# Kernel optimization log

Hardware: AMD Instinct MI355X
Metric: run time of the kernel (lower is better)

## Reference

```python
import jax, jax.numpy as jnp
import numpy as np

B, T, H, NH = 4, 4096, 768, 12
D = H          # attention inner dim (expand_ratio = 1)
I = 4 * H      # MLP intermediate size


def rms_norm(x, eps=1e-6):
    return x * jax.lax.rsqrt(jnp.mean(x * x, axis=-1, keepdims=True) + eps)


def layer_norm(x, eps=1e-6):
    mu = jnp.mean(x, axis=-1, keepdims=True)
    var = jnp.mean((x - mu) ** 2, axis=-1, keepdims=True)
    return (x - mu) * jax.lax.rsqrt(var + eps)


def act_quant(x):
    # per-token int8 absmax quantization (BitNet b1.58)
    scale = 127.0 / jnp.maximum(jnp.max(jnp.abs(x), axis=-1, keepdims=True), 1e-5)
    return jnp.clip(jnp.round(x * scale), -128, 127) / scale


def weight_quant(w):
    # per-tensor ternary quantization
    scale = 1.0 / jnp.maximum(jnp.mean(jnp.abs(w)), 1e-5)
    return jnp.clip(jnp.round(w * scale), -1, 1) / scale


def bit_linear(x, w, b=None):
    xn = rms_norm(x)
    xq = xn + jax.lax.stop_gradient(act_quant(xn) - xn)  # STE
    wq = w + jax.lax.stop_gradient(weight_quant(w) - w)  # STE
    y = jnp.einsum('...k,nk->...n', xq, wq)
    return y if b is None else y + b


def setup_inputs() -> dict:
    key = jax.random.key(0)
    ks = jax.random.split(key, 12)
    s = 0.02
    return dict(
        x=jax.random.normal(ks[0], (B, T, H), jnp.float32),
        c=jax.random.normal(ks[1], (B, H), jnp.float32),
        w_emb=jax.random.normal(ks[2], (2 * H, H), jnp.float32) * s,
        b_emb=jnp.zeros((2 * H,), jnp.float32),
        w_i=jax.random.normal(ks[3], (D, H), jnp.float32) * s,
        w_f=jax.random.normal(ks[4], (D, H), jnp.float32) * s,
        w_g=jax.random.normal(ks[5], (D, H), jnp.float32) * s,
        w_gn=jnp.ones((D,), jnp.float32),
        w_o=jax.random.normal(ks[6], (H, D), jnp.float32) * s,
        w_gate=jax.random.normal(ks[7], (2 * I, H), jnp.float32) * s,
        w_down=jax.random.normal(ks[8], (H, I), jnp.float32) * s,
        w_proj=jax.random.normal(ks[9], (H, 2 * H), jnp.float32) * s,
        b_proj=jnp.zeros((H,), jnp.float32),
    )


def reference(x, c, w_emb, b_emb, w_i, w_f, w_g, w_gn, w_o,
              w_gate, w_down, w_proj, b_proj):
    # --- AdaLayerNormZeroSingle ---
    emb = jnp.einsum('bk,nk->bn', jax.nn.silu(c), w_emb) + b_emb   # [B, 2H]
    scale, gate = jnp.split(emb, 2, axis=-1)                        # [B, H] each
    nx = layer_norm(x) * (1.0 + scale[:, None, :])                  # [B, T, H]

    # --- HGRNBitAttention: gated elementwise linear recurrence ---
    i = bit_linear(nx, w_i)                                         # [B, T, D]
    f = jax.nn.sigmoid(bit_linear(nx, w_f))                         # forget gate
    i = jax.nn.silu(i) * (1.0 - f)                                  # input gate

    def step(h, inp):
        it, ft = inp
        h = ft * h + it
        return h, h

    h0 = jnp.zeros((x.shape[0], i.shape[-1]), x.dtype)
    _, o = jax.lax.scan(step, h0, (jnp.swapaxes(i, 0, 1), jnp.swapaxes(f, 0, 1)))
    o = jnp.swapaxes(o, 0, 1)                                       # [B, T, D]

    g = bit_linear(nx, w_g)
    o = rms_norm(o) * w_gn * jax.nn.silu(g)                         # RMSNorm swish gate
    attn_out = bit_linear(o, w_o)                                   # [B, T, H]

    # --- HGRNBitMLP ---
    y = bit_linear(nx, w_gate)                                      # [B, T, 2I]
    g_m, y = jnp.split(y, 2, axis=-1)
    mlp_out = bit_linear(jax.nn.silu(g_m) * y, w_down)              # [B, T, H]

    # --- concat, project, gate, residual ---
    hs = jnp.concatenate([attn_out, mlp_out], axis=-1)              # [B, T, 2H]
    hs = gate[:, None, :] * bit_linear(hs, w_proj, b_proj)
    return x + hs
```

## Files before the change

kernel.cpp:

```cpp
#include <hip/hip_runtime.h>
#include <hip/hip_bf16.h>
#include <stdint.h>

#define HD 768
#define BB 4
#define TT 4096
#define NT (BB*TT)
#define IM 3072
#define NCH 128
#define CHL (TT/NCH)
#define MCH 4
#define MCT (NT/MCH)

typedef int v4i __attribute__((ext_vector_type(4)));
typedef __hip_bfloat16 bf16;
typedef unsigned int uint32;

__device__ __forceinline__ float wave_sum(float v){
#pragma unroll
  for (int o=32;o;o>>=1) v += __shfl_down(v,o);
  return v;
}
__device__ __forceinline__ float wave_sum_x(float v){
#pragma unroll
  for (int o=32;o;o>>=1) v += __shfl_xor(v,o);
  return v;
}
__device__ __forceinline__ float wave_max_x(float v){
#pragma unroll
  for (int o=32;o;o>>=1) v = fmaxf(v,__shfl_xor(v,o));
  return v;
}
__device__ __forceinline__ float block_sum(float v, float* lds){
  const int nw = blockDim.x >> 6;
  v = wave_sum(v);
  if ((threadIdx.x&63)==0) lds[threadIdx.x>>6] = v;
  __syncthreads();
  float r = lds[0];
  for (int i=1;i<nw;++i) r += lds[i];
  __syncthreads();
  return r;
}
__device__ __forceinline__ float sigmoidf_(float x){ return __builtin_amdgcn_rcpf(1.f + __expf(-x)); }
__device__ __forceinline__ float siluf_(float x){ return x * __builtin_amdgcn_rcpf(1.f + __expf(-x)); }
__device__ __forceinline__ float b2f(bf16 v){ return __bfloat162float(v); }
__device__ __forceinline__ bf16  f2b(float v){ return __float2bfloat16(v); }
__device__ __forceinline__ float bfb2f(uint32 u16){ uint32 v = u16<<16; return __builtin_bit_cast(float, v); }
__device__ __forceinline__ uint16_t packq2(float q0, float q1){
  int a = (int)q0, b = (int)q1;
  return (uint16_t)((a&0xff) | ((b&0xff)<<8));
}
__device__ __forceinline__ uint32 packq4(float a, float b, float c, float d){
  return (uint32)((int)a&0xff) | (((uint32)((int)b&0xff))<<8) |
         (((uint32)((int)c&0xff))<<16) | (((uint32)((int)d&0xff))<<24);
}
__device__ __forceinline__ uint32 pack2bf(float a, float b){
  uint32 ua = __builtin_bit_cast(uint16_t, f2b(a));
  uint32 ub = __builtin_bit_cast(uint16_t, f2b(b));
  return ua | (ub<<16);
}
__device__ __forceinline__ float clampq(float v){ return fminf(fmaxf(v,-128.f),127.f); }
__device__ __forceinline__ void gl_lds16(const int8_t* g, void* l){
  __builtin_amdgcn_global_load_lds((const __attribute__((address_space(1))) void*)g,
                                   (__attribute__((address_space(3))) void*)l, 16, 0, 0);
}

struct WArgs { const float* p[7]; int n[7]; size_t off[7]; };

#define WC1 589824
#define WC2 1179648
#define WC3 1769472
#define WC4 2359296
#define WC5 7077888
#define WC6 9437184
#define WCT 10616832

__global__ __launch_bounds__(256) void absum_part_all(WArgs wa, float* __restrict__ part){
  __shared__ float lds[8];
  const int seg = blockIdx.y;
  const int n4 = wa.n[seg] >> 2;
  const float4* w = (const float4*)wa.p[seg];
  float s = 0.f;
  for (int i = blockIdx.x*256 + threadIdx.x; i < n4; i += gridDim.x*256){
    float4 v = w[i];
    s += (fabsf(v.x)+fabsf(v.y)) + (fabsf(v.z)+fabsf(v.w));
  }
  s = block_sum(s, lds);
  if (threadIdx.x==0) part[seg*64 + blockIdx.x] = s;
}
__global__ __launch_bounds__(512) void absum_final_all(const float* __restrict__ part, WArgs wa,
                                                       float* __restrict__ wscv, float* __restrict__ wrec){
  int seg = threadIdx.x >> 6, lane = threadIdx.x & 63;
  float v = (seg < 7) ? part[seg*64 + lane] : 0.f;
  v = wave_sum(v);
  if (seg < 7 && lane == 0){
    float m = fmaxf(v / (float)wa.n[seg], 1e-5f);
    wscv[seg] = m; wrec[seg] = 1.f/m;
  }
}
__global__ __launch_bounds__(256) void wquant_all(WArgs wa, const float* __restrict__ wrec,
                                                  int8_t* __restrict__ q){
  const int seg = blockIdx.y;
  const int n4 = wa.n[seg] >> 2;
  const float4* p = (const float4*)wa.p[seg];
  uint32* qo = (uint32*)(q + wa.off[seg]);
  const float rc = wrec[seg];
  for (int i = blockIdx.x*256 + threadIdx.x; i < n4; i += gridDim.x*256){
    float4 v = p[i];
    int a  = (int)fminf(fmaxf(rintf(v.x*rc),-1.f),1.f);
    int b  = (int)fminf(fmaxf(rintf(v.y*rc),-1.f),1.f);
    int cc = (int)fminf(fmaxf(rintf(v.z*rc),-1.f),1.f);
    int d  = (int)fminf(fmaxf(rintf(v.w*rc),-1.f),1.f);
    qo[i] = (uint32)(a&0xff) | ((uint32)(b&0xff)<<8) | ((uint32)(cc&0xff)<<16) | ((uint32)(d&0xff)<<24);
  }
}

__global__ __launch_bounds__(256) void ada_emb(const float* __restrict__ c, const float* __restrict__ w_emb,
                                               const float* __restrict__ b_emb,
                                               float* __restrict__ scaleA, float* __restrict__ gateA){
  int o = blockIdx.x*4 + (threadIdx.x>>6);
  int lane = threadIdx.x & 63;
  int b = o / 1536, n = o % 1536;
  const float* cr = c + b*HD;
  const float* wr = w_emb + (size_t)n*HD;
  float s = 0.f;
  for (int k=lane; k<HD; k+=64){
    float cv = cr[k];
    s += siluf_(cv)*wr[k];
  }
  s = wave_sum(s);
  if (lane==0){
    s += b_emb[n];
    if (n < HD) scaleA[b*HD+n] = s;
    else        gateA[b*HD+(n-HD)] = s;
  }
}

__global__ __launch_bounds__(256) void ln_quant(const float* __restrict__ x, const float* __restrict__ scaleA,
                                                int8_t* __restrict__ xq, float* __restrict__ rsx){
  const int tok  = blockIdx.x*4 + (threadIdx.x>>6);
  const int lane = threadIdx.x & 63;
  const int b = tok >> 12;
  const float4* xr = (const float4*)(x + (size_t)tok*HD);
  const float4* sr = (const float4*)(scaleA + (size_t)b*HD);
  float4 v[3];
  float s1 = 0.f, s2 = 0.f;
#pragma unroll
  for (int j=0;j<3;++j){
    v[j] = xr[lane + j*64];
    s1 += (v[j].x+v[j].y)+(v[j].z+v[j].w);
    s2 += (v[j].x*v[j].x+v[j].y*v[j].y)+(v[j].z*v[j].z+v[j].w*v[j].w);
  }
  s1 = wave_sum_x(s1); s2 = wave_sum_x(s2);
  const float mu  = s1 * (1.f/768.f);
  const float var = fmaxf(s2 * (1.f/768.f) - mu*mu, 0.f);
  const float r1  = rsqrtf(var + 1e-6f);
  float sv[12]; float ms = 0.f, amr = 0.f;
#pragma unroll
  for (int j=0;j<3;++j){
    float4 sc = sr[lane + j*64];
    float a0 = (v[j].x-mu)*r1*(1.f+sc.x);
    float a1 = (v[j].y-mu)*r1*(1.f+sc.y);
    float a2 = (v[j].z-mu)*r1*(1.f+sc.z);
    float a3 = (v[j].w-mu)*r1*(1.f+sc.w);
    sv[4*j]=a0; sv[4*j+1]=a1; sv[4*j+2]=a2; sv[4*j+3]=a3;
    ms += (a0*a0+a1*a1)+(a2*a2+a3*a3);
    amr = fmaxf(amr, fmaxf(fmaxf(fabsf(a0),fabsf(a1)),fmaxf(fabsf(a2),fabsf(a3))));
  }
  ms = wave_sum_x(ms); amr = wave_max_x(amr);
  const float r2 = rsqrtf(ms*(1.f/768.f) + 1e-6f);
  const float am = fmaxf(amr*r2, 1e-5f);
  const float sx = 127.f/am;
  uint32* qo = (uint32*)(xq + (size_t)tok*HD);
#pragma unroll
  for (int j=0;j<3;++j){
    qo[lane + j*64] = packq4(clampq(rintf(sv[4*j]*r2*sx)),   clampq(rintf(sv[4*j+1]*r2*sx)),
                             clampq(rintf(sv[4*j+2]*r2*sx)), clampq(rintf(sv[4*j+3]*r2*sx)));
  }
  if (lane==0) rsx[tok] = am*(1.f/127.f);
}

template<int C>
__global__ __launch_bounds__(256) void rms_quant_w(const uint32* __restrict__ zin, int8_t* __restrict__ q,
                                                   float* __restrict__ rs){
  const int tok  = blockIdx.x*4 + (threadIdx.x>>6);
  const int lane = threadIdx.x & 63;
  const uint32* zp = zin + (size_t)tok*C*64;
  uint32 u[C]; float ss = 0.f, amr = 0.f;
#pragma unroll
  for (int j=0;j<C;++j){
    u[j] = zp[lane + j*64];
    float a = bfb2f(u[j] & 0xffff), b = bfb2f(u[j] >> 16);
    ss += a*a + b*b;
    amr = fmaxf(amr, fmaxf(fabsf(a),fabsf(b)));
  }
  ss = wave_sum_x(ss); amr = wave_max_x(amr);
  const float r = rsqrtf(ss*(1.f/(float)(C*128)) + 1e-6f);
  const float am = fmaxf(amr*r, 1e-5f);
  const float sx = 127.f/am;
  uint16_t* qo = (uint16_t*)(q + (size_t)tok*C*128);
#pragma unroll
  for (int j=0;j<C;++j){
    float a = bfb2f(u[j] & 0xffff), b = bfb2f(u[j] >> 16);
    qo[lane + j*64] = packq2(clampq(rintf(a*r*sx)), clampq(rintf(b*r*sx)));
  }
  if (lane==0) rs[tok] = am*(1.f/127.f);
}

__global__ __launch_bounds__(256) void rms_quant_cat(const uint32* __restrict__ pa, const uint32* __restrict__ pb,
                                                     int8_t* __restrict__ q, float* __restrict__ rs){
  const int tok  = blockIdx.x*4 + (threadIdx.x>>6);
  const int lane = threadIdx.x & 63;
  const uint32* ap = pa + (size_t)tok*(HD/2);
  const uint32* bp = pb + (size_t)tok*(HD/2);
  uint32 u[12]; float ss = 0.f, amr = 0.f;
#pragma unroll
  for (int j=0;j<6;++j){
    u[j] = ap[lane + j*64];
    float a = bfb2f(u[j] & 0xffff), b = bfb2f(u[j] >> 16);
    ss += a*a + b*b;
    amr = fmaxf(amr, fmaxf(fabsf(a),fabsf(b)));
  }
#pragma unroll
  for (int j=0;j<6;++j){
    u[6+j] = bp[lane + j*64];
    float a = bfb2f(u[6+j] & 0xffff), b = bfb2f(u[6+j] >> 16);
    ss += a*a + b*b;
    amr = fmaxf(amr, fmaxf(fabsf(a),fabsf(b)));
  }
  ss = wave_sum_x(ss); amr = wave_max_x(amr);
  const float r = rsqrtf(ss*(1.f/1536.f) + 1e-6f);
  const float am = fmaxf(amr*r, 1e-5f);
  const float sx = 127.f/am;
  uint16_t* qo = (uint16_t*)(q + (size_t)tok*(2*HD));
#pragma unroll
  for (int j=0;j<6;++j){
    float a = bfb2f(u[j] & 0xffff), b = bfb2f(u[j] >> 16);
    qo[lane + j*64] = packq2(clampq(rintf(a*r*sx)), clampq(rintf(b*r*sx)));
  }
#pragma unroll
  for (int j=0;j<6;++j){
    float a = bfb2f(u[6+j] & 0xffff), b = bfb2f(u[6+j] >> 16);
    qo[384 + lane + j*64] = packq2(clampq(rintf(a*r*sx)), clampq(rintf(b*r*sx)));
  }
  if (lane==0) rs[tok] = am*(1.f/127.f);
}

__global__ __launch_bounds__(256) void gate_norm_quant(const uint32* __restrict__ o, const uint32* __restrict__ gs,
                                                       const float* __restrict__ w_gn,
                                                       int8_t* __restrict__ oq, float* __restrict__ rso){
  const int tok  = blockIdx.x*4 + (threadIdx.x>>6);
  const int lane = threadIdx.x & 63;
  const uint32* op = o  + (size_t)tok*(HD/2);
  const uint32* gp = gs + (size_t)tok*(HD/2);
  const float2* wg = (const float2*)w_gn;
  uint32 u[6]; float ms = 0.f;
#pragma unroll
  for (int j=0;j<6;++j){
    u[j] = op[lane + j*64];
    float a = bfb2f(u[j] & 0xffff), b = bfb2f(u[j] >> 16);
    ms += a*a + b*b;
  }
  ms = wave_sum_x(ms);
  const float rn = rsqrtf(ms*(1.f/768.f) + 1e-6f);
  float uu[12]; float ms2 = 0.f, amr = 0.f;
#pragma unroll
  for (int j=0;j<6;++j){
    uint32 g = gp[lane + j*64];
    float2 w = wg[lane + j*64];
    float a = bfb2f(u[j] & 0xffff)*rn*w.x*bfb2f(g & 0xffff);
    float b = bfb2f(u[j] >> 16)  *rn*w.y*bfb2f(g >> 16);
    uu[2*j]=a; uu[2*j+1]=b;
    ms2 += a*a + b*b;
    amr = fmaxf(amr, fmaxf(fabsf(a),fabsf(b)));
  }
  ms2 = wave_sum_x(ms2); amr = wave_max_x(amr);
  const float r2 = rsqrtf(ms2*(1.f/768.f) + 1e-6f);
  const float am = fmaxf(amr*r2, 1e-5f);
  const float sx = 127.f/am;
  uint16_t* qo = (uint16_t*)(oq + (size_t)tok*HD);
#pragma unroll
  for (int j=0;j<6;++j){
    qo[lane + j*64] = packq2(clampq(rintf(uu[2*j]*r2*sx)), clampq(rintf(uu[2*j+1]*r2*sx)));
  }
  if (lane==0) rso[tok] = am*(1.f/127.f);
}

__global__ __launch_bounds__(384) void scan_pass1(const uint32* __restrict__ iact, const uint32* __restrict__ fsig,
                                                  float* __restrict__ chF, float* __restrict__ chH){
  const int blk = blockIdx.x;
  const int b = blk >> 7, ch = blk & (NCH-1);
  const int t0 = b*TT + ch*CHL;
  const size_t base = (size_t)t0*(HD/2) + threadIdx.x;
  float F0=1.f,F1=1.f,h0=0.f,h1=0.f;
#pragma unroll 4
  for (int s=0;s<CHL;++s){
    uint32 fu = fsig[base + (size_t)s*(HD/2)];
    uint32 iu = iact[base + (size_t)s*(HD/2)];
    float f0 = bfb2f(fu&0xffff), f1 = bfb2f(fu>>16);
    float a0 = bfb2f(iu&0xffff), a1 = bfb2f(iu>>16);
    h0 = f0*h0 + a0; h1 = f1*h1 + a1;
    F0 *= f0; F1 *= f1;
  }
  size_t cb = (size_t)blk*HD + 2*threadIdx.x;
  *(float2*)(chF + cb) = make_float2(F0,F1);
  *(float2*)(chH + cb) = make_float2(h0,h1);
}
__global__ __launch_bounds__(256) void scan_combine(float* __restrict__ chF, float* __restrict__ chH){
  const int gid = blockIdx.x*256 + threadIdx.x;
  const int b = gid / HD, d = gid % HD;
  float h = 0.f;
#pragma unroll 8
  for (int c=0;c<NCH;++c){
    size_t idx = (size_t)(b*NCH+c)*HD + d;
    float F = chF[idx], Hl = chH[idx];
    chH[idx] = h;
    h = F*h + Hl;
  }
}
__global__ __launch_bounds__(384) void scan_pass2(const uint32* iact, const uint32* __restrict__ fsig,
                                                  const float* __restrict__ chH, uint32* o){
  const int blk = blockIdx.x;
  const int b = blk >> 7, ch = blk & (NCH-1);
  const int t0 = b*TT + ch*CHL;
  const size_t base = (size_t)t0*(HD/2) + threadIdx.x;
  float2 hin = *(const float2*)(chH + (size_t)blk*HD + 2*threadIdx.x);
  float h0 = hin.x, h1 = hin.y;
#pragma unroll 4
  for (int s=0;s<CHL;++s){
    uint32 fu = fsig[base + (size_t)s*(HD/2)];
    uint32 iu = iact[base + (size_t)s*(HD/2)];
    float f0 = bfb2f(fu&0xffff), f1 = bfb2f(fu>>16);
    float a0 = bfb2f(iu&0xffff), a1 = bfb2f(iu>>16);
    h0 = f0*h0 + a0; h1 = f1*h1 + a1;
    uint16_t pa = __builtin_bit_cast(uint16_t, f2b(h0));
    uint16_t pb = __builtin_bit_cast(uint16_t, f2b(h1));
    o[base + (size_t)s*(HD/2)] = (uint32)pa | ((uint32)pb<<16);
  }
}

enum { EPI_IF=0, EPI_SILU=1, EPI_STORE=2, EPI_SWIGLU=3, EPI_PROJ=4 };

template<int EPI, bool DUAL>
__global__ __launch_bounds__(512) void gemm_i8(
    const int8_t* __restrict__ A, const float* __restrict__ rsA,
    const int8_t* __restrict__ B0, const int8_t* __restrict__ B1,
    const float* __restrict__ ws0p, const float* __restrict__ ws1p,
    int K, void* __restrict__ out0v, void* __restrict__ out1v,
    int ldOut, int colOff,
    const float* __restrict__ bias, const float* __restrict__ gateA,
    const float* __restrict__ xres)
{
  __shared__ __align__(16) uint8_t sA [2][16384];
  __shared__ __align__(16) uint8_t sB0[2][8192];
  __shared__ __align__(16) uint8_t sB1[DUAL?2:1][8192];

  const int lane = threadIdx.x & 63;
  const int wv   = threadIdx.x >> 6;
  const int m0 = blockIdx.x*256;
  const int n0 = blockIdx.y*128;
  const int wm = (wv>>1)*64;
  const int wn = (wv&1)*64;
  const int lr = lane & 15;
  const int sl = lane >> 4;

  const int8_t* gA[2]; const int8_t* gB0; const int8_t* gB1;
  int ldsOffA[2], ldsOffB;
#pragma unroll
  for (int j=0;j<2;++j){
    int q = wv*2 + j;
    int r = q*16 + (lane>>2);
    int cg = (lane&3) ^ ((r>>1)&3);
    gA[j] = A + (size_t)(m0+r)*K + cg*16;
    ldsOffA[j] = q*1024;
  }
  {
    int r = wv*16 + (lane>>2);
    int cg = (lane&3) ^ ((r>>1)&3);
    gB0 = B0 + (size_t)(n0+r)*K + cg*16;
    gB1 = DUAL ? (B1 + (size_t)(n0+r)*K + cg*16) : (const int8_t*)0;
    ldsOffB = wv*1024;
  }
  int offA[4], offB[4];
#pragma unroll
  for (int i=0;i<4;++i){
    int Ra = wm + i*16 + lr;
    offA[i] = Ra*64 + ((sl ^ ((Ra>>1)&3))<<4);
    int Rb = wn + i*16 + lr;
    offB[i] = Rb*64 + ((sl ^ ((Rb>>1)&3))<<4);
  }

  v4i acc0[4][4], acc1[4][4];
  const v4i vzero = {0,0,0,0};
#pragma unroll
  for (int i=0;i<4;++i)
#pragma unroll
    for (int j=0;j<4;++j){ acc0[i][j]=vzero; acc1[i][j]=vzero; }

  const int NTI = K >> 6;
#pragma unroll
  for (int j=0;j<2;++j) gl_lds16(gA[j], &sA[0][ldsOffA[j]]);
  gl_lds16(gB0, &sB0[0][ldsOffB]);
  if (DUAL) gl_lds16(gB1, &sB1[0][ldsOffB]);
  __syncthreads();

  int cur = 0;
  for (int t=0; t<NTI; ++t){
    if (t+1 < NTI){
      const int ko = (t+1)*64;
#pragma unroll
      for (int j=0;j<2;++j) gl_lds16(gA[j]+ko, &sA[cur^1][ldsOffA[j]]);
      gl_lds16(gB0+ko, &sB0[cur^1][ldsOffB]);
      if (DUAL) gl_lds16(gB1+ko, &sB1[cur^1][ldsOffB]);
    }
    v4i av[4], b0v[4], b1v[4];
#pragma unroll
    for (int i=0;i<4;++i){
      av[i]  = *(const v4i*)&sA [cur][offA[i]];
      b0v[i] = *(const v4i*)&sB0[cur][offB[i]];
    }
    if constexpr (DUAL){
#pragma unroll
      for (int i=0;i<4;++i) b1v[i] = *(const v4i*)&sB1[cur][offB[i]];
    }
#pragma unroll
    for (int mi=0;mi<4;++mi){
#pragma unroll
      for (int ni=0;ni<4;++ni){
        acc0[mi][ni] = __builtin_amdgcn_mfma_i32_16x16x64_i8(b0v[ni], av[mi], acc0[mi][ni], 0,0,0);
        if constexpr (DUAL)
          acc1[mi][ni] = __builtin_amdgcn_mfma_i32_16x16x64_i8(b1v[ni], av[mi], acc1[mi][ni], 0,0,0);
      }
    }
    __syncthreads();
    cur ^= 1;
  }

  const float w0 = *ws0p;
  const float w1 = DUAL ? *ws1p : 0.f;
  const int rb = sl*4;
  const int em0 = m0 + wm, en0 = n0 + wn;
#pragma unroll
  for (int mi=0;mi<4;++mi){
    const int tok = em0 + mi*16 + lr;
    const float rs = rsA[tok];
#pragma unroll
    for (int ni=0;ni<4;++ni){
      const int ch = en0 + ni*16 + rb;
      float y0[4], y1[4];
#pragma unroll
      for (int r=0;r<4;++r){
        y0[r] = (float)acc0[mi][ni][r] * rs * w0;
        if constexpr (DUAL) y1[r] = (float)acc1[mi][ni][r] * rs * w1;
      }
      if constexpr (EPI==EPI_IF){
        float fs[4], io[4];
#pragma unroll
        for (int r=0;r<4;++r){ fs[r] = sigmoidf_(y1[r]); io[r] = siluf_(y0[r])*(1.f-fs[r]); }
        uint2 ui, uf;
        ui.x = pack2bf(io[0],io[1]); ui.y = pack2bf(io[2],io[3]);
        uf.x = pack2bf(fs[0],fs[1]); uf.y = pack2bf(fs[2],fs[3]);
        *(uint2*)((bf16*)out0v + (size_t)tok*ldOut + ch) = ui;
        *(uint2*)((bf16*)out1v + (size_t)tok*ldOut + ch) = uf;
      } else if constexpr (EPI==EPI_SILU){
        uint2 u;
        u.x = pack2bf(siluf_(y0[0]), siluf_(y0[1]));
        u.y = pack2bf(siluf_(y0[2]), siluf_(y0[3]));
        *(uint2*)((bf16*)out0v + (size_t)tok*ldOut + ch) = u;
      } else if constexpr (EPI==EPI_STORE){
        uint2 u;
        u.x = pack2bf(y0[0],y0[1]); u.y = pack2bf(y0[2],y0[3]);
        *(uint2*)((bf16*)out0v + (size_t)tok*ldOut + colOff + ch) = u;
      } else if constexpr (EPI==EPI_SWIGLU){
        uint2 u;
        u.x = pack2bf(siluf_(y0[0])*y1[0], siluf_(y0[1])*y1[1]);
        u.y = pack2bf(siluf_(y0[2])*y1[2], siluf_(y0[3])*y1[3]);
        *(uint2*)((bf16*)out0v + (size_t)tok*ldOut + ch) = u;
      } else {
        const int bidx = tok >> 12;
        float4 b4 = *(const float4*)(bias + ch);
        float4 g4 = *(const float4*)(gateA + bidx*HD + ch);
        float4 x4 = *(const float4*)(xres + (size_t)tok*HD + ch);
        float4 o4;
        o4.x = x4.x + g4.x*(y0[0] + b4.x);
        o4.y = x4.y + g4.y*(y0[1] + b4.y);
        o4.z = x4.z + g4.z*(y0[2] + b4.z);
        o4.w = x4.w + g4.w*(y0[3] + b4.w);
        *(float4*)((float*)out0v + (size_t)tok*HD + ch) = o4;
      }
    }
  }
}

extern "C" void kernel_launch(void* const* d_in, const int* in_sizes, int n_in,
                              void* d_out, int out_size, void* d_ws, size_t ws_size,
                              hipStream_t stream){
  const float* x      = (const float*)d_in[0];
  const float* c      = (const float*)d_in[1];
  const float* w_emb  = (const float*)d_in[2];
  const float* b_emb  = (const float*)d_in[3];
  const float* w_i    = (const float*)d_in[4];
  const float* w_f    = (const float*)d_in[5];
  const float* w_g    = (const float*)d_in[6];
  const float* w_gn   = (const float*)d_in[7];
  const float* w_o    = (const float*)d_in[8];
  const float* w_gate = (const float*)d_in[9];
  const float* w_down = (const float*)d_in[10];
  const float* w_proj = (const float*)d_in[11];
  const float* b_proj = (const float*)d_in[12];
  float* out = (float*)d_out;
  char* ws = (char*)d_ws;

  constexpr size_t SZ_HH   = (size_t)HD*HD;
  constexpr size_t o_wq     = 0;
  constexpr size_t o_wsc    = o_wq + (size_t)WCT;
  constexpr size_t o_wrecip = o_wsc    + 256;
  constexpr size_t o_part   = o_wrecip + 256;
  constexpr size_t o_scaleA = o_part   + 2048;
  constexpr size_t o_gateA  = o_scaleA + (size_t)BB*HD*4;
  constexpr size_t o_rsx    = o_gateA  + (size_t)BB*HD*4;
  constexpr size_t o_rso    = o_rsx    + (size_t)NT*4;
  constexpr size_t o_rsh    = o_rso    + (size_t)NT*4;
  constexpr size_t o_rsm    = o_rsh    + (size_t)NT*4;
  constexpr size_t o_xq     = o_rsm    + (size_t)NT*4;
  constexpr size_t o_END0   = o_xq     + (size_t)NT*HD;

  constexpr size_t o_R1     = o_END0;
  constexpr size_t o_R2     = o_R1     + (size_t)NT*HD*2;
  constexpr size_t o_R3     = o_R2     + (size_t)NT*HD*2;
  constexpr size_t o_chF    = o_R3     + (size_t)NT*HD*2;
  constexpr size_t o_chH    = o_chF    + (size_t)BB*NCH*HD*4;
  constexpr size_t o_R4     = o_chH    + (size_t)BB*NCH*HD*4;
  constexpr size_t NEED_S   = o_R4     + (size_t)NT*HD;

  constexpr size_t o_Z      = o_END0;
  constexpr size_t o_M      = o_Z + (size_t)NT*IM*2;
  constexpr size_t o_chF2   = o_M + (size_t)NT*IM;
  constexpr size_t o_chH2   = o_chF2 + (size_t)BB*NCH*HD*4;
  constexpr size_t NEED_B   = o_chH2 + (size_t)BB*NCH*HD*4;

  if (ws_size < NEED_S) return;
  const bool big = (ws_size >= NEED_B);

  float*  wscv  = (float*)(ws + o_wsc);
  float*  wrec  = (float*)(ws + o_wrecip);
  float*  part  = (float*)(ws + o_part);
  float*  scaleA= (float*)(ws + o_scaleA);
  float*  gateA = (float*)(ws + o_gateA);
  float*  rsx   = (float*)(ws + o_rsx);
  float*  rso   = (float*)(ws + o_rso);
  float*  rsh   = (float*)(ws + o_rsh);
  float*  rsm   = (float*)(ws + o_rsm);
  int8_t* xq    = (int8_t*)(ws + o_xq);
  int8_t* wqall = (int8_t*)(ws + o_wq);
  int8_t* wqp[7] = { wqall, wqall+WC1, wqall+WC2, wqall+WC3, wqall+WC4, wqall+WC5, wqall+WC6 };

  WArgs wa;
  wa.p[0]=w_i; wa.p[1]=w_f; wa.p[2]=w_g; wa.p[3]=w_o; wa.p[4]=w_gate; wa.p[5]=w_down; wa.p[6]=w_proj;
  wa.n[0]=(int)SZ_HH; wa.n[1]=(int)SZ_HH; wa.n[2]=(int)SZ_HH; wa.n[3]=(int)SZ_HH;
  wa.n[4]=2*IM*HD; wa.n[5]=HD*IM; wa.n[6]=HD*2*HD;
  wa.off[0]=0; wa.off[1]=WC1; wa.off[2]=WC2; wa.off[3]=WC3; wa.off[4]=WC4; wa.off[5]=WC5; wa.off[6]=WC6;

  absum_part_all <<<dim3(64,7),  dim3(256), 0, stream>>>(wa, part);
  absum_final_all<<<dim3(1),     dim3(512), 0, stream>>>(part, wa, wscv, wrec);
  wquant_all     <<<dim3(256,7), dim3(256), 0, stream>>>(wa, wrec, wqall);
  ada_emb <<<dim3(1536), dim3(256), 0, stream>>>(c, w_emb, b_emb, scaleA, gateA);
  ln_quant<<<dim3(NT/4), dim3(256), 0, stream>>>(x, scaleA, xq, rsx);

  if (big){
    bf16* zc      = (bf16*)(ws + o_Z);
    bf16* iact    = (bf16*)(ws + o_Z);
    bf16* fsig    = (bf16*)(ws + o_Z + (size_t)NT*HD*2);
    bf16* gsilu   = (bf16*)(ws + o_Z + (size_t)2*NT*HD*2);
    bf16* attn    = gsilu;
    bf16* mlp     = (bf16*)(ws + o_Z + (size_t)3*NT*HD*2);
    int8_t* mq    = (int8_t*)(ws + o_M);
    int8_t* oq    = (int8_t*)(ws + o_M);
    int8_t* hq    = (int8_t*)(ws + o_M + (size_t)NT*HD);
    float* chF    = (float*)(ws + o_chF2);
    float* chH    = (float*)(ws + o_chH2);
    bf16* obuf    = iact;

    gemm_i8<EPI_SWIGLU,true><<<dim3(NT/256,24), dim3(512), 0, stream>>>(
        xq, rsx, wqp[4], wqp[4] + (size_t)IM*HD, wscv+4, wscv+4, HD,
        zc, nullptr, IM, 0, nullptr, nullptr, nullptr);
    rms_quant_w<24><<<dim3(NT/4), dim3(256), 0, stream>>>((const uint32*)zc, mq, rsm);
    gemm_i8<EPI_STORE,false><<<dim3(NT/256,6), dim3(512), 0, stream>>>(
        mq, rsm, wqp[5], nullptr, wscv+5, nullptr, IM, mlp, nullptr, HD, 0, nullptr, nullptr, nullptr);

    gemm_i8<EPI_IF,true><<<dim3(NT/256,6), dim3(512), 0, stream>>>(
        xq, rsx, wqp[0], wqp[1], wscv+0, wscv+1, HD, iact, fsig, HD, 0, nullptr, nullptr, nullptr);
    gemm_i8<EPI_SILU,false><<<dim3(NT/256,6), dim3(512), 0, stream>>>(
        xq, rsx, wqp[2], nullptr, wscv+2, nullptr, HD, gsilu, nullptr, HD, 0, nullptr, nullptr, nullptr);
    scan_pass1 <<<dim3(BB*NCH), dim3(384), 0, stream>>>((const uint32*)iact, (const uint32*)fsig, chF, chH);
    scan_combine<<<dim3(12),    dim3(256), 0, stream>>>(chF, chH);
    scan_pass2 <<<dim3(BB*NCH), dim3(384), 0, stream>>>((const uint32*)iact, (const uint32*)fsig, chH, (uint32*)obuf);
    gate_norm_quant<<<dim3(NT/4), dim3(256), 0, stream>>>((const uint32*)obuf, (const uint32*)gsilu, w_gn, oq, rso);
    gemm_i8<EPI_STORE,false><<<dim3(NT/256,6), dim3(512), 0, stream>>>(
        oq, rso, wqp[3], nullptr, wscv+3, nullptr, HD, attn, nullptr, HD, 0, nullptr, nullptr, nullptr);

    rms_quant_cat<<<dim3(NT/4), dim3(256), 0, stream>>>((const uint32*)attn, (const uint32*)mlp, hq, rsh);
    gemm_i8<EPI_PROJ,false><<<dim3(NT/256,6), dim3(512), 0, stream>>>(
        hq, rsh, wqp[6], nullptr, wscv+6, nullptr, 2*HD, out, nullptr, HD, 0, b_proj, gateA, x);
  } else {
    bf16*   iact  = (bf16*)(ws + o_R1);
    bf16*   fsig  = (bf16*)(ws + o_R2);
    bf16*   gsilu = (bf16*)(ws + o_R3);
    bf16*   obuf  = iact;
    bf16*   hs    = (bf16*)(ws + o_R1);
    bf16*   zc    = (bf16*)(ws + o_R3);
    int8_t* hq    = (int8_t*)(ws + o_R3);
    float*  chF   = (float*)(ws + o_chF);
    float*  chH   = (float*)(ws + o_chH);
    int8_t* oq    = (int8_t*)(ws + o_R4);
    int8_t* mq    = (int8_t*)(ws + o_R4);

    gemm_i8<EPI_IF,true><<<dim3(NT/256,6), dim3(512), 0, stream>>>(
        xq, rsx, wqp[0], wqp[1], wscv+0, wscv+1, HD, iact, fsig, HD, 0, nullptr, nullptr, nullptr);
    gemm_i8<EPI_SILU,false><<<dim3(NT/256,6), dim3(512), 0, stream>>>(
        xq, rsx, wqp[2], nullptr, wscv+2, nullptr, HD, gsilu, nullptr, HD, 0, nullptr, nullptr, nullptr);
    scan_pass1 <<<dim3(BB*NCH), dim3(384), 0, stream>>>((const uint32*)iact, (const uint32*)fsig, chF, chH);
    scan_combine<<<dim3(12),    dim3(256), 0, stream>>>(chF, chH);
    scan_pass2 <<<dim3(BB*NCH), dim3(384), 0, stream>>>((const uint32*)iact, (const uint32*)fsig, chH, (uint32*)obuf);
    gate_norm_quant<<<dim3(NT/4), dim3(256), 0, stream>>>((const uint32*)obuf, (const uint32*)gsilu, w_gn, oq, rso);
    gemm_i8<EPI_STORE,false><<<dim3(NT/256,6), dim3(512), 0, stream>>>(
        oq, rso, wqp[3], nullptr, wscv+3, nullptr, HD, hs, nullptr, 2*HD, 0, nullptr, nullptr, nullptr);
    for (int cc=0; cc<MCH; ++cc){
      const size_t r0 = (size_t)cc*MCT;
      gemm_i8<EPI_SWIGLU,true><<<dim3(MCT/256,24), dim3(512), 0, stream>>>(
          xq + r0*HD, rsx + r0, wqp[4], wqp[4] + (size_t)IM*HD, wscv+4, wscv+4, HD,
          zc, nullptr, IM, 0, nullptr, nullptr, nullptr);
      rms_quant_w<24><<<dim3(MCT/4), dim3(256), 0, stream>>>((const uint32*)zc, mq, rsm);
      gemm_i8<EPI_STORE,false><<<dim3(MCT/256,6), dim3(512), 0, stream>>>(
          mq, rsm, wqp[5], nullptr, wscv+5, nullptr, IM,
          hs + r0*2*HD, nullptr, 2*HD, HD, nullptr, nullptr, nullptr);
    }
    rms_quant_w<12><<<dim3(NT/4), dim3(256), 0, stream>>>((const uint32*)hs, hq, rsh);
    gemm_i8<EPI_PROJ,false><<<dim3(NT/256,6), dim3(512), 0, stream>>>(
        hq, rsh, wqp[6], nullptr, wscv+6, nullptr, 2*HD, out, nullptr, HD, 0, b_proj, gateA, x);
  }

  (void)in_sizes; (void)n_in; (void)out_size;
}
```

Baseline: 459.0 us.

## Software-pipeline int8 GEMM main loop with register double buffering and explicit waitcnts

Restructures the int8 MFMA GEMM K-loop so LDS reads for the next tile are issued before the MFMAs of the current tile, using two register buffer sets and a two-step unrolled loop. Global-to-LDS loads are staged two tiles ahead, with hand-written s_waitcnt vmcnt/lgkmcnt and raw s_barrier in place of __syncthreads. MFMA sections are wrapped in s_setprio to favour matrix issue, and sched_barrier fixes the instruction order. The aim is to hide LDS read and global load latency behind MFMA work. In exchange it uses more registers, and it assumes NTI is even and that the vmcnt values match the exact number of outstanding loads.

```diff
diff --git a/kernel.cpp b/kernel.cpp
--- a/kernel.cpp
+++ b/kernel.cpp
@@ -398,43 +398,89 @@
     for (int j=0;j<4;++j){ acc0[i][j]=vzero; acc1[i][j]=vzero; }
 
   const int NTI = K >> 6;
-#pragma unroll
-  for (int j=0;j<2;++j) gl_lds16(gA[j], &sA[0][ldsOffA[j]]);
-  gl_lds16(gB0, &sB0[0][ldsOffB]);
-  if (DUAL) gl_lds16(gB1, &sB1[0][ldsOffB]);
-  __syncthreads();
-
-  int cur = 0;
-  for (int t=0; t<NTI; ++t){
-    if (t+1 < NTI){
-      const int ko = (t+1)*64;
-#pragma unroll
-      for (int j=0;j<2;++j) gl_lds16(gA[j]+ko, &sA[cur^1][ldsOffA[j]]);
-      gl_lds16(gB0+ko, &sB0[cur^1][ldsOffB]);
-      if (DUAL) gl_lds16(gB1+ko, &sB1[cur^1][ldsOffB]);
+
+#define STAGE(KO, BUF) do { \
+    _Pragma("unroll") \
+    for (int j_=0;j_<2;++j_) gl_lds16(gA[j_]+(KO), &sA[BUF][ldsOffA[j_]]); \
+    gl_lds16(gB0+(KO), &sB0[BUF][ldsOffB]); \
+    if constexpr (DUAL) gl_lds16(gB1+(KO), &sB1[BUF][ldsOffB]); \
+  } while(0)
+
+#define DSREAD(BUF, AV, B0V, B1V) do { \
+    _Pragma("unroll") \
+    for (int i_=0;i_<4;++i_){ \
+      AV[i_]  = *(const v4i*)&sA [BUF][offA[i_]]; \
+      B0V[i_] = *(const v4i*)&sB0[BUF][offB[i_]]; \
+    } \
+    if constexpr (DUAL){ \
+      _Pragma("unroll") \
+      for (int i_=0;i_<4;++i_) B1V[i_] = *(const v4i*)&sB1[BUF][offB[i_]]; \
+    } \
+  } while(0)
+
+#define MMA(AV, B0V, B1V) do { \
+    __builtin_amdgcn_s_setprio(1); \
+    _Pragma("unroll") \
+    for (int mi_=0;mi_<4;++mi_){ \
+      _Pragma("unroll") \
+      for (int ni_=0;ni_<4;++ni_){ \
+        acc0[mi_][ni_] = __builtin_amdgcn_mfma_i32_16x16x64_i8(B0V[ni_], AV[mi_], acc0[mi_][ni_], 0,0,0); \
+        if constexpr (DUAL) \
+          acc1[mi_][ni_] = __builtin_amdgcn_mfma_i32_16x16x64_i8(B1V[ni_], AV[mi_], acc1[mi_][ni_], 0,0,0); \
+      } \
+    } \
+    __builtin_amdgcn_s_setprio(0); \
+  } while(0)
+
+#define WAIT_VM_LD() do { \
+    if constexpr (DUAL) asm volatile("s_waitcnt vmcnt(4)" ::: "memory"); \
+    else                asm volatile("s_waitcnt vmcnt(3)" ::: "memory"); \
+  } while(0)
+
+  v4i av0[4], b00[4], b10[4];
+  v4i av1[4], b01[4], b11[4];
+
+  STAGE(0, 0);
+  STAGE(64, 1);
+  WAIT_VM_LD();
+  asm volatile("s_barrier" ::: "memory");
+  DSREAD(0, av0, b00, b10);
+  asm volatile("s_waitcnt lgkmcnt(0)" ::: "memory");
+  asm volatile("s_barrier" ::: "memory");
+
+  for (int t=0; t<NTI; t+=2){
+    const bool last = (t+2 >= NTI);
+    if (!last){
+      STAGE((t+2)*64, 0);
+      WAIT_VM_LD();
+    } else {
+      asm volatile("s_waitcnt vmcnt(0)" ::: "memory");
     }
-    v4i av[4], b0v[4], b1v[4];
-#pragma unroll
-    for (int i=0;i<4;++i){
-      av[i]  = *(const v4i*)&sA [cur][offA[i]];
-      b0v[i] = *(const v4i*)&sB0[cur][offB[i]];
+    asm volatile("s_barrier" ::: "memory");
+    DSREAD(1, av1, b01, b11);
+    __builtin_amdgcn_sched_barrier(0);
+    MMA(av0, b00, b10);
+    asm volatile("s_waitcnt lgkmcnt(0)" ::: "memory");
+    asm volatile("s_barrier" ::: "memory");
+    if (!last){
+      STAGE((t+3)*64, 1);
+      WAIT_VM_LD();
+      asm volatile("s_barrier" ::: "memory");
+      DSREAD(0, av0, b00, b10);
+      __builtin_amdgcn_sched_barrier(0);
+      MMA(av1, b01, b11);
+      asm volatile("s_waitcnt lgkmcnt(0)" ::: "memory");
+      asm volatile("s_barrier" ::: "memory");
+    } else {
+      __builtin_amdgcn_sched_barrier(0);
+      MMA(av1, b01, b11);
     }
-    if constexpr (DUAL){
-#pragma unroll
-      for (int i=0;i<4;++i) b1v[i] = *(const v4i*)&sB1[cur][offB[i]];
-    }
-#pragma unroll
-    for (int mi=0;mi<4;++mi){
-#pragma unroll
-      for (int ni=0;ni<4;++ni){
-        acc0[mi][ni] = __builtin_amdgcn_mfma_i32_16x16x64_i8(b0v[ni], av[mi], acc0[mi][ni], 0,0,0);
-        if constexpr (DUAL)
-          acc1[mi][ni] = __builtin_amdgcn_mfma_i32_16x16x64_i8(b1v[ni], av[mi], acc1[mi][ni], 0,0,0);
-      }
-    }
-    __syncthreads();
-    cur ^= 1;
-  }
+  }
+
+#undef STAGE
+#undef DSREAD
+#undef MMA
+#undef WAIT_VM_LD
 
   const float w0 = *ws0p;
   const float w1 = DUAL ? *ws1p : 0.f;
```

After: 1.707 ms. 272% more time.

## Interleave LDS reads with MFMA rows using barriers, sched fences and setprio

Applied to the files above, without the earlier changes.

Restructures the int8 GEMM main loop so that LDS fragment reads for each A row are interleaved with MFMA bursts. Explicit s_barrier, sched_barrier and s_setprio calls keep waves in a ping-pong rhythm, and the global-to-LDS prefetch is issued right after the first fragment reads. The aim is to overlap LDS latency with matrix-core work and to give MFMA-issuing waves priority. The cost is many extra barriers per K tile, plus hand-placed vmcnt waits that serialise the warps more tightly.

```diff
diff --git a/kernel.cpp b/kernel.cpp
--- a/kernel.cpp
+++ b/kernel.cpp
@@ -398,43 +398,92 @@
     for (int j=0;j<4;++j){ acc0[i][j]=vzero; acc1[i][j]=vzero; }
 
   const int NTI = K >> 6;
-#pragma unroll
-  for (int j=0;j<2;++j) gl_lds16(gA[j], &sA[0][ldsOffA[j]]);
-  gl_lds16(gB0, &sB0[0][ldsOffB]);
-  if (DUAL) gl_lds16(gB1, &sB1[0][ldsOffB]);
-  __syncthreads();
+
+#define STAGE(KO, BUF) do { \
+    _Pragma("unroll") \
+    for (int j_=0;j_<2;++j_) gl_lds16(gA[j_]+(KO), &sA[BUF][ldsOffA[j_]]); \
+    gl_lds16(gB0+(KO), &sB0[BUF][ldsOffB]); \
+    if constexpr (DUAL) gl_lds16(gB1+(KO), &sB1[BUF][ldsOffB]); \
+  } while(0)
+
+#define RD_B(BUF) do { \
+    _Pragma("unroll") \
+    for (int i_=0;i_<4;++i_) b0v[i_] = *(const v4i*)&sB0[BUF][offB[i_]]; \
+    if constexpr (DUAL){ \
+      _Pragma("unroll") \
+      for (int i_=0;i_<4;++i_) b1v[i_] = *(const v4i*)&sB1[BUF][offB[i_]]; \
+    } \
+  } while(0)
+
+#define MMA_ROW(MI) do { \
+    __builtin_amdgcn_s_setprio(1); \
+    _Pragma("unroll") \
+    for (int ni_=0;ni_<4;++ni_){ \
+      acc0[MI][ni_] = __builtin_amdgcn_mfma_i32_16x16x64_i8(b0v[ni_], av[MI], acc0[MI][ni_], 0,0,0); \
+      if constexpr (DUAL) \
+        acc1[MI][ni_] = __builtin_amdgcn_mfma_i32_16x16x64_i8(b1v[ni_], av[MI], acc1[MI][ni_], 0,0,0); \
+    } \
+    __builtin_amdgcn_s_setprio(0); \
+  } while(0)
+
+#define BAR() asm volatile("s_barrier" ::: "memory")
+#define SB()  __builtin_amdgcn_sched_barrier(0)
+
+  STAGE(0, 0);
+  asm volatile("s_waitcnt vmcnt(0)" ::: "memory");
+  BAR();
 
   int cur = 0;
+  v4i av[4], b0v[4], b1v[4];
   for (int t=0; t<NTI; ++t){
-    if (t+1 < NTI){
-      const int ko = (t+1)*64;
-#pragma unroll
-      for (int j=0;j<2;++j) gl_lds16(gA[j]+ko, &sA[cur^1][ldsOffA[j]]);
-      gl_lds16(gB0+ko, &sB0[cur^1][ldsOffB]);
-      if (DUAL) gl_lds16(gB1+ko, &sB1[cur^1][ldsOffB]);
+    const bool more = (t+1 < NTI);
+    if constexpr (DUAL){
+      RD_B(cur);
+      av[0] = *(const v4i*)&sA[cur][offA[0]];
+      if (more) STAGE((t+1)*64, cur^1);
+      BAR(); SB();
+      MMA_ROW(0);
+      SB(); BAR();
+      av[1] = *(const v4i*)&sA[cur][offA[1]];
+      BAR(); SB();
+      MMA_ROW(1);
+      SB(); BAR();
+      av[2] = *(const v4i*)&sA[cur][offA[2]];
+      BAR(); SB();
+      MMA_ROW(2);
+      SB(); BAR();
+      av[3] = *(const v4i*)&sA[cur][offA[3]];
+      BAR(); SB();
+      MMA_ROW(3);
+      SB();
+      if (more) asm volatile("s_waitcnt vmcnt(0)" ::: "memory");
+      BAR();
+    } else {
+      RD_B(cur);
+      av[0] = *(const v4i*)&sA[cur][offA[0]];
+      av[1] = *(const v4i*)&sA[cur][offA[1]];
+      if (more) STAGE((t+1)*64, cur^1);
+      BAR(); SB();
+      MMA_ROW(0);
+      MMA_ROW(1);
+      SB(); BAR();
+      av[2] = *(const v4i*)&sA[cur][offA[2]];
+      av[3] = *(const v4i*)&sA[cur][offA[3]];
+      BAR(); SB();
+      MMA_ROW(2);
+      MMA_ROW(3);
+      SB();
+      if (more) asm volatile("s_waitcnt vmcnt(0)" ::: "memory");
+      BAR();
     }
-    v4i av[4], b0v[4], b1v[4];
-#pragma unroll
-    for (int i=0;i<4;++i){
-      av[i]  = *(const v4i*)&sA [cur][offA[i]];
-      b0v[i] = *(const v4i*)&sB0[cur][offB[i]];
-    }
-    if constexpr (DUAL){
-#pragma unroll
-      for (int i=0;i<4;++i) b1v[i] = *(const v4i*)&sB1[cur][offB[i]];
-    }
-#pragma unroll
-    for (int mi=0;mi<4;++mi){
-#pragma unroll
-      for (int ni=0;ni<4;++ni){
-        acc0[mi][ni] = __builtin_amdgcn_mfma_i32_16x16x64_i8(b0v[ni], av[mi], acc0[mi][ni], 0,0,0);
-        if constexpr (DUAL)
-          acc1[mi][ni] = __builtin_amdgcn_mfma_i32_16x16x64_i8(b1v[ni], av[mi], acc1[mi][ni], 0,0,0);
-      }
-    }
-    __syncthreads();
     cur ^= 1;
   }
+
+#undef STAGE
+#undef RD_B
+#undef MMA_ROW
+#undef BAR
+#undef SB
 
   const float w0 = *ws0p;
   const float w1 = DUAL ? *ws1p : 0.f;
```

Measured after the change: 471.1 us. 2.6% more time.
